# Performance work log

Hardware: AMD Instinct MI355X
Metric: run time of the kernel (lower is better)

## Reference

```python
import jax, jax.numpy as jnp
import numpy as np

TEMP = 0.07
HARD_K = 512
EMB_D = 768
PROJ_D = 128
QUEUE = 32768
BATCH = 2048
NUM_CLASSES = 2


def setup_inputs() -> dict:
    key = jax.random.key(0)
    ks = jax.random.split(key, 8)
    embeddings = jax.random.normal(ks[0], (BATCH, EMB_D), dtype=jnp.float32)
    labels = jax.random.randint(ks[1], (BATCH,), 0, NUM_CLASSES)
    # projector params: Linear(D,D) -> ReLU -> Linear(D,128)
    W1 = jax.random.normal(ks[2], (EMB_D, EMB_D), dtype=jnp.float32) * 0.02
    b1 = jnp.zeros((EMB_D,), dtype=jnp.float32)
    W2 = jax.random.normal(ks[3], (EMB_D, PROJ_D), dtype=jnp.float32) * 0.02
    b2 = jnp.zeros((PROJ_D,), dtype=jnp.float32)
    # queue buffers: L2-normalized random embeddings (as in __init__) with valid labels
    qe = jax.random.normal(ks[4], (QUEUE, PROJ_D), dtype=jnp.float32)
    queue_embeddings = qe / jnp.linalg.norm(qe, axis=1, keepdims=True)
    queue_labels = jax.random.randint(ks[5], (QUEUE,), 0, NUM_CLASSES)
    return {
        'embeddings': embeddings, 'labels': labels,
        'W1': W1, 'b1': b1, 'W2': W2, 'b2': b2,
        'queue_embeddings': queue_embeddings, 'queue_labels': queue_labels,
    }


def reference(embeddings, labels, W1, b1, W2, b2, queue_embeddings, queue_labels):
    n = embeddings.shape[0]
    # projector + L2 normalize
    h = jax.nn.relu(embeddings @ W1 + b1)
    z = h @ W2 + b2
    z = z / jnp.linalg.norm(z, axis=1, keepdims=True)  # (N, 128)

    # pairwise in-batch similarities, scaled by temperature
    S = (z @ z.T) / TEMP  # (N, N)
    same = labels[:, None] == labels[None, :]
    eye = jnp.eye(n, dtype=bool)
    pos_mask = same & ~eye           # positives: same label, not self
    neg_mask = ~same                 # in-batch negatives: different label

    # logsumexp over in-batch negatives per anchor (-inf rows -> -inf, handled by logaddexp)
    neg_batch = jnp.where(neg_mask, S, -jnp.inf)
    lse_batch = jax.scipy.special.logsumexp(neg_batch, axis=1)  # (N,)

    # hard negatives from queue: opposite-label, top-K by similarity
    sims_q = z @ queue_embeddings.T  # (N, Q)
    opp = (queue_labels[None, :] != labels[:, None]) & (queue_labels[None, :] >= 0)
    masked_q = jnp.where(opp, sims_q, -jnp.inf)
    topk_vals, _ = jax.lax.top_k(masked_q, HARD_K)  # (N, K); -inf pads drop from logsumexp
    # fallback (no opposite-label entries): first K queue embeddings regardless of label
    fallback = sims_q[:, :HARD_K]
    has_opp = opp.any(axis=1, keepdims=True)
    neg_q = jnp.where(has_opp, topk_vals, fallback) / TEMP
    lse_queue = jax.scipy.special.logsumexp(neg_q, axis=1)  # (N,)

    # all negatives for anchor i: batch negatives ++ queue hard negatives
    lse_neg = jnp.logaddexp(lse_batch, lse_queue)  # (N,)

    # per positive pair (i, j): log_prob = pos_sim - logsumexp([pos_sim, negs])
    log_prob = S - jnp.logaddexp(S, lse_neg[:, None])  # (N, N)
    losses = jnp.where(pos_mask, -log_prob, 0.0)
    count = pos_mask.sum()
    return jnp.where(count > 0, losses.sum() / count.astype(losses.dtype), 0.0)
```

## Files before the change

kernel.cpp:

```cpp
#include <hip/hip_runtime.h>
#include <hip/hip_fp16.h>

#define BATCH_N   2048
#define EMB_D_    768
#define PROJ_D_   128
#define QUEUE_N   32768
#define HARD_K_   512
static constexpr float INV_T  = 1.0f / 0.07f;
static constexpr float WLO    = 0.12f;
static constexpr float S8ENC  = 255.0f / 0.88f;
static constexpr float BINW   = 0.88f / 255.0f;

typedef __attribute__((ext_vector_type(8))) short short8;
typedef __attribute__((ext_vector_type(4))) short short4v;
typedef __attribute__((ext_vector_type(4))) float f32x4;

__device__ __forceinline__ unsigned short f2bf(float f) {
    unsigned u = __float_as_uint(f);
    unsigned r = u + 0x7fffu + ((u >> 16) & 1u);
    return (unsigned short)(r >> 16);
}
__device__ __forceinline__ float bf2f(short s) {
    return __uint_as_float(((unsigned)(unsigned short)s) << 16);
}
__device__ __forceinline__ int opp_of(int mylab, const int* __restrict__ qcnt) {
    const int same = (mylab == 0) ? qcnt[0] : ((mylab == 1) ? qcnt[1] : 0);
    return qcnt[2] - same;
}

__global__ void __launch_bounds__(256) prep(const float* __restrict__ emb, short* __restrict__ embb,
                                            const float* __restrict__ queue, short* __restrict__ qb,
                                            const int* __restrict__ qlab, int* __restrict__ qpart,
                                            const float* __restrict__ W1, short* __restrict__ w1t,
                                            const float* __restrict__ W2, short* __restrict__ w2t,
                                            const int* __restrict__ labels, int* __restrict__ rcnt,
                                            int* __restrict__ pc) {
    __shared__ float tile[64][65];
    const int b = blockIdx.x, t = threadIdx.x;
    if (b < 1536) {
        const int i = b * 256 + t;
        const float4 f = ((const float4*)emb)[i];
        short4v o = {(short)f2bf(f.x), (short)f2bf(f.y), (short)f2bf(f.z), (short)f2bf(f.w)};
        ((short4v*)embb)[i] = o;
    } else if (b < 5632) {
        const int i = (b - 1536) * 256 + t;
        const float4 f = ((const float4*)queue)[i];
        short4v o = {(short)f2bf(f.x), (short)f2bf(f.y), (short)f2bf(f.z), (short)f2bf(f.w)};
        ((short4v*)qb)[i] = o;
    } else if (b < 5664) {
        const int i = (b - 5632) * 256 + t;
        int c0 = 0, c1 = 0, cv = 0;
        for (int j = i; j < QUEUE_N; j += 8192) {
            const int q = qlab[j];
            c0 += (q == 0); c1 += (q == 1); cv += (q >= 0);
        }
        #pragma unroll
        for (int o = 32; o > 0; o >>= 1) {
            c0 += __shfl_xor(c0, o); c1 += __shfl_xor(c1, o); cv += __shfl_xor(cv, o);
        }
        int* red = (int*)tile;
        const int wv = t >> 6;
        if ((t & 63) == 0) { red[wv * 4 + 0] = c0; red[wv * 4 + 1] = c1; red[wv * 4 + 2] = cv; }
        __syncthreads();
        if (t == 0) {
            const int bb = (b - 5632) * 4;
            qpart[bb + 0] = red[0] + red[4] + red[8]  + red[12];
            qpart[bb + 1] = red[1] + red[5] + red[9]  + red[13];
            qpart[bb + 2] = red[2] + red[6] + red[10] + red[14];
        }
    } else if (b < 5832) {
        const int bid = b - 5664;
        const float* A; short* At; int R, C, bx, by;
        if (bid < 144) { A = W1; At = w1t; R = EMB_D_; C = EMB_D_;  bx = (bid % 12) * 64; by = (bid / 12) * 64; }
        else { const int b2 = bid - 144; A = W2; At = w2t; R = EMB_D_; C = PROJ_D_; bx = (b2 & 1) * 64; by = (b2 >> 1) * 64; }
        const int tc = t & 63, tg = t >> 6;
        #pragma unroll
        for (int i = 0; i < 16; i++) {
            const int r = tg * 16 + i;
            tile[r][tc] = A[(size_t)(by + r) * C + bx + tc];
        }
        __syncthreads();
        #pragma unroll
        for (int i = 0; i < 16; i++) {
            const int r = tg * 16 + i;
            At[(size_t)(bx + r) * R + by + tc] = (short)f2bf(tile[tc][r]);
        }
    } else {
        int c = 0;
        for (int j = t; j < BATCH_N; j += 256) c += (labels[j] == 0);
        #pragma unroll
        for (int o = 32; o > 0; o >>= 1) c += __shfl_xor(c, o);
        int* red = (int*)tile;
        if ((t & 63) == 0) red[t >> 6] = c;
        __syncthreads();
        if (t == 0) rcnt[0] = red[0] + red[1] + red[2] + red[3];
        if (t < 8) pc[t] = 0;
    }
}

__global__ void __launch_bounds__(256) mfma_h64(const short* __restrict__ Ab,
                                                const short* __restrict__ Bb,
                                                const float* __restrict__ bias,
                                                short* __restrict__ C,
                                                int N, int K) {
    __shared__ __align__(16) short As[64 * 128];
    __shared__ __align__(16) short Bs[128 * 128];
    const int t = threadIdx.x;
    const int lane = t & 63, wv = t >> 6;
    const int l16 = lane & 15, l4 = lane >> 4;
    const int m0 = blockIdx.y * 64, n0 = blockIdx.x * 128;
    const int wn = wv * 32;

    f32x4 acc[4][2];
    #pragma unroll
    for (int i = 0; i < 4; ++i)
        #pragma unroll
        for (int j = 0; j < 2; ++j) acc[i][j] = f32x4{0.f, 0.f, 0.f, 0.f};

    for (int kb = 0; kb < K; kb += 128) {
        __syncthreads();
        #pragma unroll
        for (int it = 0; it < 4; ++it) {
            const int r = it * 4 + wv, row = r * 4 + l4, cg = l16 ^ (row & 15);
            __builtin_amdgcn_global_load_lds(
                (const __attribute__((address_space(1))) void*)(Ab + (size_t)(m0 + row) * K + kb + cg * 8),
                (__attribute__((address_space(3))) void*)(As + r * 512), 16, 0, 0);
        }
        #pragma unroll
        for (int it = 0; it < 8; ++it) {
            const int r = it * 4 + wv, row = r * 4 + l4, cg = l16 ^ (row & 15);
            __builtin_amdgcn_global_load_lds(
                (const __attribute__((address_space(1))) void*)(Bb + (size_t)(n0 + row) * K + kb + cg * 8),
                (__attribute__((address_space(3))) void*)(Bs + r * 512), 16, 0, 0);
        }
        __syncthreads();
        #pragma unroll
        for (int ks = 0; ks < 4; ++ks) {
            short8 af[4], bfr[2];
            const int ch = (ks * 4 + l4) ^ l16;
            #pragma unroll
            for (int i = 0; i < 4; ++i)
                af[i] = *(const short8*)(As + (i * 16 + l16) * 128 + ch * 8);
            #pragma unroll
            for (int j = 0; j < 2; ++j)
                bfr[j] = *(const short8*)(Bs + (wn + j * 16 + l16) * 128 + ch * 8);
            #pragma unroll
            for (int i = 0; i < 4; ++i)
                #pragma unroll
                for (int j = 0; j < 2; ++j)
                    acc[i][j] = __builtin_amdgcn_mfma_f32_16x16x32_bf16(af[i], bfr[j], acc[i][j], 0, 0, 0);
        }
    }

    float bsv[2];
    #pragma unroll
    for (int j = 0; j < 2; ++j) bsv[j] = bias[n0 + wn + j * 16 + l16];
    #pragma unroll
    for (int i = 0; i < 4; ++i)
        #pragma unroll
        for (int r = 0; r < 4; ++r) {
            const int m = m0 + i * 16 + l4 * 4 + r;
            #pragma unroll
            for (int j = 0; j < 2; ++j) {
                const int n = n0 + wn + j * 16 + l16;
                const float v = fmaxf(acc[i][j][r] + bsv[j], 0.0f);
                C[(size_t)m * N + n] = (short)f2bf(v);
            }
        }
}

__global__ void __launch_bounds__(256) znorm_perm(const short* __restrict__ Ab,
                                                  const short* __restrict__ Bb,
                                                  const float* __restrict__ bias,
                                                  short* __restrict__ zb,
                                                  const int* __restrict__ qlab,
                                                  const int* __restrict__ labels,
                                                  const int* __restrict__ qpart,
                                                  const int* __restrict__ rcnt,
                                                  int* __restrict__ qcnt,
                                                  int* __restrict__ colidx,
                                                  int* __restrict__ qlabp,
                                                  int* __restrict__ rowmap,
                                                  int* __restrict__ rlabp,
                                                  int* __restrict__ pc) {
    __shared__ __align__(16) short As[32 * 128];
    __shared__ __align__(16) short Bs[128 * 128];
    __shared__ float ssq[32];
    __shared__ int wcnt[4][3];
    __shared__ int gbase[3];
    const int blk = blockIdx.x;
    const int t = threadIdx.x;
    const int lane = t & 63, wv = t >> 6;

    if (blk >= 64) {
        const unsigned long long below = (1ull << lane) - 1ull;
        int q0 = 0, q1 = 0, qv = 0;
        for (int i = 0; i < 32; ++i) {
            q0 += qpart[i * 4]; q1 += qpart[i * 4 + 1]; qv += qpart[i * 4 + 2];
        }
        if (blk < 192) {
            const int cb = blk - 64;
            if (cb == 0 && t == 0) { qcnt[0] = q0; qcnt[1] = q1; qcnt[2] = qv; }
            const int j = cb * 256 + t;
            const int q = qlab[j];
            const int cls = (q == 0) ? 0 : ((q == 1) ? 1 : 2);
            const unsigned long long b0 = __ballot(cls == 0);
            const unsigned long long b1 = __ballot(cls == 1);
            const unsigned long long b2 = __ballot(cls == 2);
            const int rank = (cls == 0) ? __popcll(b0 & below)
                           : ((cls == 1) ? __popcll(b1 & below) : __popcll(b2 & below));
            if (lane == 0) {
                wcnt[wv][0] = __popcll(b0); wcnt[wv][1] = __popcll(b1); wcnt[wv][2] = __popcll(b2);
            }
            __syncthreads();
            if (t < 3) {
                const int tot = wcnt[0][t] + wcnt[1][t] + wcnt[2][t] + wcnt[3][t];
                gbase[t] = atomicAdd(&pc[t], tot);
            }
            __syncthreads();
            int wb = 0;
            #pragma unroll
            for (int w = 0; w < 4; ++w) if (w < wv) wb += wcnt[w][cls];
            const int cbase = (cls == 0) ? 0 : ((cls == 1) ? q0 : q0 + q1);
            const int pos = cbase + gbase[cls] + wb + rank;
            colidx[pos] = j; qlabp[pos] = q;
        } else {
            const int r = (blk - 192) * 256 + t;
            const int l = labels[r];
            const int cls = (l == 0) ? 0 : 1;
            const unsigned long long b0 = __ballot(cls == 0);
            const unsigned long long b1 = __ballot(cls == 1);
            const int rank = (cls == 0) ? __popcll(b0 & below) : __popcll(b1 & below);
            if (lane == 0) { wcnt[wv][0] = __popcll(b0); wcnt[wv][1] = __popcll(b1); }
            __syncthreads();
            if (t < 2) {
                const int tot = wcnt[0][t] + wcnt[1][t] + wcnt[2][t] + wcnt[3][t];
                gbase[t] = atomicAdd(&pc[3 + t], tot);
            }
            __syncthreads();
            int wb = 0;
            #pragma unroll
            for (int w = 0; w < 4; ++w) if (w < wv) wb += wcnt[w][cls];
            const int cbase = (cls == 0) ? 0 : rcnt[0];
            const int pos = cbase + gbase[cls] + wb + rank;
            rowmap[pos] = r; rlabp[pos] = l;
        }
        return;
    }

    const int l16 = lane & 15, l4 = lane >> 4;
    const int m0 = blk * 32;
    const int wn = wv * 32;
    const int K = EMB_D_;

    if (t < 32) ssq[t] = 0.0f;

    f32x4 acc[2][2];
    #pragma unroll
    for (int i = 0; i < 2; ++i)
        #pragma unroll
        for (int j = 0; j < 2; ++j) acc[i][j] = f32x4{0.f, 0.f, 0.f, 0.f};

    for (int kb = 0; kb < K; kb += 128) {
        __syncthreads();
        #pragma unroll
        for (int it = 0; it < 2; ++it) {
            const int r = it * 4 + wv, row = r * 4 + l4, cg = l16 ^ (row & 15);
            __builtin_amdgcn_global_load_lds(
                (const __attribute__((address_space(1))) void*)(Ab + (size_t)(m0 + row) * K + kb + cg * 8),
                (__attribute__((address_space(3))) void*)(As + r * 512), 16, 0, 0);
        }
        #pragma unroll
        for (int it = 0; it < 8; ++it) {
            const int r = it * 4 + wv, row = r * 4 + l4, cg = l16 ^ (row & 15);
            __builtin_amdgcn_global_load_lds(
                (const __attribute__((address_space(1))) void*)(Bb + (size_t)(row) * K + kb + cg * 8),
                (__attribute__((address_space(3))) void*)(Bs + r * 512), 16, 0, 0);
        }
        __syncthreads();
        #pragma unroll
        for (int ks = 0; ks < 4; ++ks) {
            short8 af[2], bfr[2];
            const int ch = (ks * 4 + l4) ^ l16;
            #pragma unroll
            for (int i = 0; i < 2; ++i)
                af[i] = *(const short8*)(As + (i * 16 + l16) * 128 + ch * 8);
            #pragma unroll
            for (int j = 0; j < 2; ++j)
                bfr[j] = *(const short8*)(Bs + (wn + j * 16 + l16) * 128 + ch * 8);
            #pragma unroll
            for (int i = 0; i < 2; ++i)
                #pragma unroll
                for (int j = 0; j < 2; ++j)
                    acc[i][j] = __builtin_amdgcn_mfma_f32_16x16x32_bf16(af[i], bfr[j], acc[i][j], 0, 0, 0);
        }
    }

    float bsv[2];
    #pragma unroll
    for (int j = 0; j < 2; ++j) bsv[j] = bias[wn + j * 16 + l16];
    #pragma unroll
    for (int i = 0; i < 2; ++i)
        #pragma unroll
        for (int r = 0; r < 4; ++r) {
            float p = 0.0f;
            #pragma unroll
            for (int j = 0; j < 2; ++j) {
                acc[i][j][r] += bsv[j];
                p += acc[i][j][r] * acc[i][j][r];
            }
            #pragma unroll
            for (int o = 8; o > 0; o >>= 1) p += __shfl_xor(p, o);
            if (l16 == 0) atomicAdd(&ssq[i * 16 + l4 * 4 + r], p);
        }
    __syncthreads();
    #pragma unroll
    for (int i = 0; i < 2; ++i)
        #pragma unroll
        for (int r = 0; r < 4; ++r) {
            const int lrow = i * 16 + l4 * 4 + r;
            const float inv = rsqrtf(ssq[lrow]);
            #pragma unroll
            for (int j = 0; j < 2; ++j)
                zb[(size_t)(m0 + lrow) * PROJ_D_ + wn + j * 16 + l16] =
                    (short)f2bf(acc[i][j][r] * inv);
        }
}

__global__ void __launch_bounds__(256) mask8_spack(const short* __restrict__ zb,
                                                   const short* __restrict__ qb,
                                                   unsigned char* __restrict__ codes,
                                                   const int* __restrict__ rlabp,
                                                   const int* __restrict__ qlabp,
                                                   const int* __restrict__ colidx,
                                                   const int* __restrict__ rowmap,
                                                   const int* __restrict__ qcnt,
                                                   const int* __restrict__ rcnt,
                                                   short* __restrict__ Sbuf) {
    __shared__ __align__(16) short As[64 * 128];
    __shared__ __align__(16) short Bs[128 * 128];
    const int bid = blockIdx.x, t = threadIdx.x;
    const int lane = t & 63, wv = t >> 6;
    const int l16 = lane & 15, l4 = lane >> 4;
    const int wm = (wv & 1) * 32, wn = (wv >> 1) * 64;

    if (bid >= 2048) {
        const int q = bid - 2048;
        const int m0 = (q >> 4) * 64, n0 = (q & 15) * 128;
        #pragma unroll
        for (int it = 0; it < 4; ++it) {
            const int r = it * 4 + wv, row = r * 4 + l4, cg = l16 ^ (row & 15);
            __builtin_amdgcn_global_load_lds(
                (const __attribute__((address_space(1))) void*)(zb + (size_t)(m0 + row) * 128 + cg * 8),
                (__attribute__((address_space(3))) void*)(As + r * 512), 16, 0, 0);
        }
        #pragma unroll
        for (int it = 0; it < 8; ++it) {
            const int r = it * 4 + wv, row = r * 4 + l4, cg = l16 ^ (row & 15);
            __builtin_amdgcn_global_load_lds(
                (const __attribute__((address_space(1))) void*)(zb + (size_t)(n0 + row) * 128 + cg * 8),
                (__attribute__((address_space(3))) void*)(Bs + r * 512), 16, 0, 0);
        }
        __syncthreads();

        f32x4 acc[2][4];
        #pragma unroll
        for (int i = 0; i < 2; ++i)
            #pragma unroll
            for (int j = 0; j < 4; ++j) acc[i][j] = f32x4{0.f, 0.f, 0.f, 0.f};

        #pragma unroll
        for (int ks = 0; ks < 4; ++ks) {
            short8 af[2], bfr[4];
            const int ch = (ks * 4 + l4) ^ l16;
            #pragma unroll
            for (int i = 0; i < 2; ++i)
                af[i]  = *(const short8*)(As + (wm + i * 16 + l16) * 128 + ch * 8);
            #pragma unroll
            for (int j = 0; j < 4; ++j)
                bfr[j] = *(const short8*)(Bs + (wn + j * 16 + l16) * 128 + ch * 8);
            #pragma unroll
            for (int i = 0; i < 2; ++i)
                #pragma unroll
                for (int j = 0; j < 4; ++j)
                    acc[i][j] = __builtin_amdgcn_mfma_f32_16x16x32_bf16(af[i], bfr[j], acc[i][j], 0, 0, 0);
        }
        #pragma unroll
        for (int i = 0; i < 2; ++i)
            #pragma unroll
            for (int r = 0; r < 4; ++r) {
                const int m = m0 + wm + i * 16 + l4 * 4 + r;
                union { unsigned short u[4]; uint2 d; } pk;
                #pragma unroll
                for (int j = 0; j < 4; ++j) pk.u[j] = f2bf(acc[i][j][r]);
                *(uint2*)(Sbuf + (size_t)m * BATCH_N + n0 + wn + l16 * 4) = pk.d;
            }
        return;
    }

    const int bx = bid & 63, by = bid >> 6;
    const int m0 = by * 64;
    const int c0 = qcnt[0], c1v = qcnt[1], r0 = rcnt[0];
    int lo, hi;
    if (m0 + 64 <= r0)  { lo = c0; hi = c0 + c1v; }
    else if (m0 >= r0)  { lo = 0;  hi = c0; }
    else                { lo = 0;  hi = c0 + c1v; }
    const int bs = bx * 512;
    if (bs + 512 <= lo || bs >= hi) return;

    int ra[4], ca[32], la[8], qa[16];
    #pragma unroll
    for (int it = 0; it < 4; ++it)
        ra[it] = rowmap[m0 + (it * 4 + wv) * 4 + l4];
    #pragma unroll
    for (int tt = 0; tt < 4; ++tt)
        #pragma unroll
        for (int it = 0; it < 8; ++it)
            ca[tt * 8 + it] = colidx[bs + tt * 128 + (it * 4 + wv) * 4 + l4];
    #pragma unroll
    for (int i = 0; i < 2; ++i)
        #pragma unroll
        for (int r = 0; r < 4; ++r)
            la[i * 4 + r] = rlabp[m0 + wm + i * 16 + l4 * 4 + r];
    #pragma unroll
    for (int tt = 0; tt < 4; ++tt)
        #pragma unroll
        for (int j = 0; j < 4; ++j)
            qa[tt * 4 + j] = qlabp[bs + tt * 128 + wn + j * 16 + l16];

    #pragma unroll
    for (int it = 0; it < 4; ++it) {
        const int r = it * 4 + wv, row = r * 4 + l4, cg = l16 ^ (row & 15);
        __builtin_amdgcn_global_load_lds(
            (const __attribute__((address_space(1))) void*)(zb + (size_t)ra[it] * 128 + cg * 8),
            (__attribute__((address_space(3))) void*)(As + r * 512), 16, 0, 0);
    }
    #pragma unroll
    for (int it = 0; it < 8; ++it) {
        const int r = it * 4 + wv, row = r * 4 + l4, cg = l16 ^ (row & 15);
        __builtin_amdgcn_global_load_lds(
            (const __attribute__((address_space(1))) void*)(qb + (size_t)ca[it] * 128 + cg * 8),
            (__attribute__((address_space(3))) void*)(Bs + r * 512), 16, 0, 0);
    }
    const float C0 = 1.0f - WLO * S8ENC;
    __syncthreads();

    #pragma unroll
    for (int tt = 0; tt < 4; ++tt) {
        const int n0 = bs + tt * 128;

        f32x4 acc[2][4];
        #pragma unroll
        for (int i = 0; i < 2; ++i)
            #pragma unroll
            for (int j = 0; j < 4; ++j) acc[i][j] = f32x4{0.f, 0.f, 0.f, 0.f};

        #pragma unroll
        for (int ks = 0; ks < 4; ++ks) {
            short8 af[2], bfr[4];
            const int ch = (ks * 4 + l4) ^ l16;
            #pragma unroll
            for (int i = 0; i < 2; ++i)
                af[i]  = *(const short8*)(As + (wm + i * 16 + l16) * 128 + ch * 8);
            #pragma unroll
            for (int j = 0; j < 4; ++j)
                bfr[j] = *(const short8*)(Bs + (wn + j * 16 + l16) * 128 + ch * 8);
            #pragma unroll
            for (int i = 0; i < 2; ++i)
                #pragma unroll
                for (int j = 0; j < 4; ++j)
                    acc[i][j] = __builtin_amdgcn_mfma_f32_16x16x32_bf16(af[i], bfr[j], acc[i][j], 0, 0, 0);
        }

        if (tt < 3) {
            __syncthreads();
            #pragma unroll
            for (int it = 0; it < 8; ++it) {
                const int r = it * 4 + wv, row = r * 4 + l4, cg = l16 ^ (row & 15);
                __builtin_amdgcn_global_load_lds(
                    (const __attribute__((address_space(1))) void*)(qb + (size_t)ca[(tt + 1) * 8 + it] * 128 + cg * 8),
                    (__attribute__((address_space(3))) void*)(Bs + r * 512), 16, 0, 0);
            }
        }

        float a0[4], a1[4];
        #pragma unroll
        for (int j = 0; j < 4; ++j) {
            const int q = qa[tt * 4 + j];
            a0[j] = (q >= 0 && q != 0) ? C0 : -1e9f;
            a1[j] = (q >= 0 && q != 1) ? C0 : -1e9f;
        }
        #pragma unroll
        for (int i = 0; i < 2; ++i) {
            #pragma unroll
            for (int r = 0; r < 4; ++r) {
                const int m  = m0 + wm + i * 16 + l4 * 4 + r;
                const bool z = (la[i * 4 + r] == 0);
                unsigned pk = 0;
                #pragma unroll
                for (int j = 0; j < 4; ++j) {
                    const float add = z ? a0[j] : a1[j];
                    const float f = fmaf(acc[i][j][r], S8ENC, add);
#if __has_builtin(__builtin_amdgcn_cvt_pk_u8_f32)
                    pk = __builtin_amdgcn_cvt_pk_u8_f32(f, j, pk);
#else
                    const unsigned c = (unsigned)fminf(fmaxf(f, 0.0f), 255.0f);
                    pk |= c << (8 * j);
#endif
                }
                *(unsigned*)(codes + (size_t)m * QUEUE_N + n0 + wn + l16 * 4) = pk;
            }
        }
        if (tt < 3) __syncthreads();
    }
}

__device__ __forceinline__ void find_crossing(int* hist, int* grp, int target,
                                              int* s_bin, int* s_chi) {
    const int t = threadIdx.x;
    const int b0 = hist[4*t], b1 = hist[4*t+1], b2 = hist[4*t+2], b3 = hist[4*t+3];
    grp[t] = b0 + b1 + b2 + b3;
    __syncthreads();
    for (int off = 1; off < 256; off <<= 1) {
        int add = (t + off < 256) ? grp[t + off] : 0;
        __syncthreads();
        grp[t] += add;
        __syncthreads();
    }
    int cab = (t < 255) ? grp[t + 1] : 0;
    const int hb[4] = {b0, b1, b2, b3};
    #pragma unroll
    for (int i = 3; i >= 0; i--) {
        const int h = hb[i];
        if (cab < target && cab + h >= target) { *s_bin = 4*t + i; *s_chi = cab; }
        cab += h;
    }
    __syncthreads();
}

#define FOR_ALL_VALS(BODY)                                                   \
    _Pragma("unroll")                                                        \
    for (int _k = 0; _k < 64; _k++) {                                        \
        const float2 _f = __half22float2(*(const __half2*)&dv[_k]);          \
        { const float v = _f.x; BODY }                                       \
        { const float v = _f.y; BODY }                                       \
    }

__global__ void __launch_bounds__(256) tail_row(const unsigned char* __restrict__ codes,
                                                const int* __restrict__ qcnt,
                                                const int* __restrict__ rlabp,
                                                const int* __restrict__ rowmap,
                                                const short* __restrict__ zb,
                                                const short* __restrict__ qb,
                                                const int* __restrict__ qlab,
                                                const short* __restrict__ S,
                                                const int* __restrict__ labels,
                                                float* __restrict__ part_out,
                                                int* __restrict__ cnt_out) {
    __shared__ int hist4[1024];
    __shared__ int grp[256];
    __shared__ float zrow[128];
    __shared__ int s_bin, s_chi, s_bin2, s_chi2;
    __shared__ float scf[4];
    __shared__ int sci[4];
    __shared__ float s_Lq;
    const int p = blockIdx.x, t = threadIdx.x;
    const int orig  = rowmap[p];
    const int myLab = rlabp[p];
    const int opp   = opp_of(myLab, qcnt);

    bool have = false;
    if (opp >= HARD_K_) {
        for (int k = t; k < 1024; k += 256) hist4[k] = 0;
        __syncthreads();

        const int c0 = qcnt[0];
        const int lo = (myLab == 0) ? c0 : 0;
        const int hi = (myLab == 0) ? c0 + qcnt[1] : c0;
        const int klo = (lo & ~511) >> 4;
        const int khi = ((hi + 511) & ~511) >> 4;

        int* myh = hist4 + (t >> 6) * 256;
        const uint4* rowp = (const uint4*)(codes + (size_t)p * QUEUE_N);
        for (int k = klo + t; k < khi; k += 256) {
            const uint4 u = rowp[k];
            const unsigned w[4] = {u.x, u.y, u.z, u.w};
            #pragma unroll
            for (int q = 0; q < 4; q++)
                #pragma unroll
                for (int s = 0; s < 4; s++) {
                    const int c = (w[q] >> (8 * s)) & 0xFF;
                    if (c) atomicAdd(&myh[c], 1);
                }
        }
        __syncthreads();
        const int h = hist4[t] + hist4[256 + t] + hist4[512 + t] + hist4[768 + t];
        grp[t] = h;
        __syncthreads();
        for (int off = 1; off < 256; off <<= 1) {
            int add = (t + off < 256) ? grp[t + off] : 0;
            __syncthreads();
            grp[t] += add;
            __syncthreads();
        }
        const int total = grp[1];
        have = (total >= HARD_K_);
        if (have) {
            {
                const int above = (t < 255) ? grp[t + 1] : 0;
                if (grp[t] >= HARD_K_ && above < HARD_K_) s_bin = t;
            }
            __syncthreads();
            const int b = s_bin;

            float e = 0.0f;
            if (t > b && h) e = (float)h * __expf((WLO + ((float)t - 0.5f) * BINW - 1.0f) * INV_T);
            #pragma unroll
            for (int o = 32; o > 0; o >>= 1) e += __shfl_xor(e, o);
            if ((t & 63) == 0) scf[t >> 6] = e;
            __syncthreads();
            if (t == 0) {
                const float Eab  = scf[0] + scf[1] + scf[2] + scf[3];
                const int   cab  = (b < 255) ? grp[b + 1] : 0;
                const float ebin = __expf((WLO + ((float)b - 0.5f) * BINW - 1.0f) * INV_T);
                const float sadj = Eab + (float)(HARD_K_ - cab) * ebin;
                s_Lq = INV_T + __logf(sadj);
            }
        } else {
            __syncthreads();
        }
    }

    if (!have) {
        int* fh = hist4;
        if (t < 128) zrow[t] = bf2f(zb[(size_t)orig * 128 + t]);
        __syncthreads();

        const int mylab = myLab;
        unsigned dv[64];
        float rm = -1e30f, rs = 0.0f;
        for (int k = 0; k < 128; k++) {
            const int j = t + 256 * k;
            float d = 0.0f;
            #pragma unroll
            for (int c = 0; c < 16; ++c) {
                const short8 qv = *(const short8*)(qb + (size_t)j * 128 + c * 8);
                #pragma unroll
                for (int e = 0; e < 8; ++e) d += zrow[c * 8 + e] * bf2f(qv[e]);
            }
            if (j < HARD_K_) {
                const float sv = d * INV_T;
                if (sv > rm) { rs = rs * __expf(rm - sv) + 1.0f; rm = sv; }
                else         { rs += __expf(sv - rm); }
            }
            const int q = qlab[j];
            const float mv = (q != mylab && q >= 0) ? d : -65504.0f;
            const __half h = __float2half(mv);
            unsigned short* pp = (unsigned short*)&dv[k >> 1];
            pp[k & 1] = *(const unsigned short*)&h;
        }

        if (opp == 0) {
            float rm2 = rm, rs2 = rs;
            #pragma unroll
            for (int o = 32; o > 0; o >>= 1) {
                const float om = __shfl_xor(rm2, o), os = __shfl_xor(rs2, o);
                const float nm = fmaxf(rm2, om);
                rs2 = rs2 * __expf(rm2 - nm) + os * __expf(om - nm);
                rm2 = nm;
            }
            if ((t & 63) == 0) { scf[t >> 6] = rm2; ((float*)sci)[t >> 6] = rs2; }
            __syncthreads();
            if (t == 0) {
                float M = -1e30f, Sx = 0.0f;
                for (int w = 0; w < 4; w++) {
                    const float nm = fmaxf(M, scf[w]);
                    Sx = Sx * __expf(M - nm) + ((float*)sci)[w] * __expf(scf[w] - nm);
                    M = nm;
                }
                s_Lq = M + __logf(Sx);
            }
        } else if (opp < HARD_K_) {
            float mm = -1e30f, ss = 0.0f;
            FOR_ALL_VALS(
                if (v > -60000.0f) {
                    const float sv = v * INV_T;
                    if (sv > mm) { ss = ss * __expf(mm - sv) + 1.0f; mm = sv; }
                    else         { ss += __expf(sv - mm); }
                } )
            #pragma unroll
            for (int o = 32; o > 0; o >>= 1) {
                const float om = __shfl_xor(mm, o), os = __shfl_xor(ss, o);
                const float nm = fmaxf(mm, om);
                ss = ss * __expf(mm - nm) + os * __expf(om - nm);
                mm = nm;
            }
            if ((t & 63) == 0) { scf[t >> 6] = mm; ((float*)sci)[t >> 6] = ss; }
            __syncthreads();
            if (t == 0) {
                float M = -1e30f, Sx = 0.0f;
                for (int w = 0; w < 4; w++) {
                    const float nm = fmaxf(M, scf[w]);
                    Sx = Sx * __expf(M - nm) + ((float*)sci)[w] * __expf(scf[w] - nm);
                    M = nm;
                }
                s_Lq = M + __logf(Sx);
            }
        } else {
            float mloc = -1e30f;
            FOR_ALL_VALS( mloc = fmaxf(mloc, v); )
            #pragma unroll
            for (int o = 32; o > 0; o >>= 1) mloc = fmaxf(mloc, __shfl_xor(mloc, o));
            if ((t & 63) == 0) scf[t >> 6] = mloc;
            __syncthreads();
            const float m = fmaxf(fmaxf(scf[0], scf[1]), fmaxf(scf[2], scf[3]));

            int c1 = 0, c2 = 0;
            const float w1 = m - 0.25f, w2 = m - 1.0f;
            FOR_ALL_VALS( c1 += (v >= w1); c2 += (v >= w2); )
            #pragma unroll
            for (int o = 32; o > 0; o >>= 1) { c1 += __shfl_xor(c1, o); c2 += __shfl_xor(c2, o); }
            if ((t & 63) == 0) { sci[t >> 6] = c1; }
            __syncthreads();
            const int C1 = sci[0] + sci[1] + sci[2] + sci[3];
            __syncthreads();
            if ((t & 63) == 0) { sci[t >> 6] = c2; }
            __syncthreads();
            const int C2 = sci[0] + sci[1] + sci[2] + sci[3];

            float lo;
            if      (C1 >= HARD_K_) lo = w1;
            else if (C2 >= HARD_K_) lo = w2;
            else                    lo = -1.01f;
            const float range = m - lo;
            const float scale = 1024.0f / range;

            for (int k = t; k < 1024; k += 256) fh[k] = 0;
            __syncthreads();
            FOR_ALL_VALS(
                if (v >= lo) {
                    const float bf = fminf((v - lo) * scale, 1023.0f);
                    atomicAdd(&fh[(int)bf], 1);
                } )
            __syncthreads();
            find_crossing(fh, grp, HARD_K_, &s_bin, &s_chi);
            const int   bin1 = s_bin, chi1 = s_chi;
            const float binw = range * (1.0f / 1024.0f);
            const float lo1  = lo + bin1 * binw;
            const float ssc  = 1024.0f / binw;

            for (int k = t; k < 1024; k += 256) fh[k] = 0;
            __syncthreads();
            FOR_ALL_VALS(
                if (v >= lo) {
                    const float bf = fminf((v - lo) * scale, 1023.0f);
                    if ((int)bf == bin1) {
                        const float sf = fminf(fmaxf((v - lo1) * ssc, 0.0f), 1023.0f);
                        atomicAdd(&fh[(int)sf], 1);
                    }
                } )
            __syncthreads();
            find_crossing(fh, grp, HARD_K_ - chi1, &s_bin2, &s_chi2);
            const float thr = lo1 + s_bin2 * (binw * (1.0f / 1024.0f));

            float sl = 0.0f; int cg = 0;
            FOR_ALL_VALS( if (v > thr) { cg++; sl += __expf((v - m) * INV_T); } )
            #pragma unroll
            for (int o = 32; o > 0; o >>= 1) { sl += __shfl_xor(sl, o); cg += __shfl_xor(cg, o); }
            if ((t & 63) == 0) { scf[t >> 6] = sl; sci[t >> 6] = cg; }
            __syncthreads();
            if (t == 0) {
                const float slt = scf[0] + scf[1] + scf[2] + scf[3];
                const int   cgt = sci[0] + sci[1] + sci[2] + sci[3];
                const float sadj = slt + ((float)HARD_K_ - (float)cgt) * __expf((thr - m) * INV_T);
                s_Lq = m * INV_T + __logf(sadj);
            }
        }
    }
    __syncthreads();

    if (t >= 64) return;
    const int lane = t;
    const uint4* rp = (const uint4*)(S + (size_t)orig * BATCH_N);

    float v[32]; int lb[32];
    #pragma unroll
    for (int kk = 0; kk < 4; kk++) {
        const uint4 u = rp[lane + 64 * kk];
        const unsigned w[4] = {u.x, u.y, u.z, u.w};
        const int base = (lane + 64 * kk) * 8;
        #pragma unroll
        for (int q = 0; q < 4; q++) {
            v[kk * 8 + 2 * q]     = __uint_as_float(w[q] << 16);
            v[kk * 8 + 2 * q + 1] = __uint_as_float(w[q] & 0xFFFF0000u);
            const int i0 = base + 2 * q, i1 = base + 2 * q + 1;
            lb[kk * 8 + 2 * q]     = labels[(i0 & ~63) + ((i0 & 3) << 4) + ((i0 >> 2) & 15)];
            lb[kk * 8 + 2 * q + 1] = labels[(i1 & ~63) + ((i1 & 3) << 4) + ((i1 >> 2) & 15)];
        }
    }

    const float REF = INV_T;
    float sneg = 0.0f;
    #pragma unroll
    for (int k = 0; k < 32; k++) {
        const float ev = __expf(v[k] * INV_T - REF);
        sneg += (lb[k] != myLab) ? ev : 0.0f;
    }
    #pragma unroll
    for (int o = 32; o > 0; o >>= 1) sneg += __shfl_xor(sneg, o);
    const float lseb = (sneg > 0.0f) ? REF + __logf(sneg) : -1e30f;
    const float Lq = s_Lq;
    const float mx0 = fmaxf(lseb, Lq), mn0 = fminf(lseb, Lq);
    const float L = mx0 + __logf(1.0f + __expf(mn0 - mx0));

    float part = 0.0f; int cnt = 0;
    #pragma unroll
    for (int k = 0; k < 32; k++) {
        const int idx = ((lane + 64 * (k >> 3)) * 8) + (k & 7);
        const int col = (idx & ~63) + ((idx & 3) << 4) + ((idx >> 2) & 15);
        if (lb[k] == myLab && col != orig) {
            const float sv = v[k] * INV_T;
            const float mx = fmaxf(sv, L), mn = fminf(sv, L);
            part += (mx - sv) + __logf(1.0f + __expf(mn - mx));
            cnt++;
        }
    }
    #pragma unroll
    for (int o = 32; o > 0; o >>= 1) { part += __shfl_xor(part, o); cnt += __shfl_xor(cnt, o); }
    if (lane == 0) { part_out[orig] = part; cnt_out[orig] = cnt; }
}

__global__ void __launch_bounds__(256) finalize_loss(const float* __restrict__ part,
                                                     const int* __restrict__ cnt,
                                                     float* __restrict__ out) {
    const int t = threadIdx.x;
    float s = 0.0f; int c = 0;
    #pragma unroll
    for (int k = 0; k < 8; k++) { s += part[t + 256 * k]; c += cnt[t + 256 * k]; }
    #pragma unroll
    for (int o = 32; o > 0; o >>= 1) { s += __shfl_xor(s, o); c += __shfl_xor(c, o); }
    __shared__ float sf[4]; __shared__ int sc[4];
    if ((t & 63) == 0) { sf[t >> 6] = s; sc[t >> 6] = c; }
    __syncthreads();
    if (t == 0) {
        const float st = sf[0] + sf[1] + sf[2] + sf[3];
        const int   ct = sc[0] + sc[1] + sc[2] + sc[3];
        out[0] = (ct > 0) ? (st / (float)ct) : 0.0f;
    }
}

extern "C" void kernel_launch(void* const* d_in, const int* in_sizes, int n_in,
                              void* d_out, int out_size, void* d_ws, size_t ws_size,
                              hipStream_t stream) {
    const float* emb    = (const float*)d_in[0];
    const int*   labels = (const int*)  d_in[1];
    const float* W1     = (const float*)d_in[2];
    const float* b1     = (const float*)d_in[3];
    const float* W2     = (const float*)d_in[4];
    const float* b2     = (const float*)d_in[5];
    const float* queue  = (const float*)d_in[6];
    const int*   qlab   = (const int*)  d_in[7];

    char* ws = (char*)d_ws;
    short*         Sbuf  = (short*)        (ws);
    unsigned char* codes = (unsigned char*)(ws + 16777216);
    short*         embb  = (short*)        (ws + 83886080);
    short*         hbf   = (short*)        (ws + 87031808);
    short*         zb    = (short*)        (ws + 90177536);
    short*         qb    = (short*)        (ws + 90701824);
    short*         w1t   = (short*)        (ws + 99090432);
    short*         w2t   = (short*)        (ws + 100270080);
    int*           qcnt  = (int*)          (ws + 100474880);
    int*           rcnt  = (int*)          (ws + 100474944);
    int*           pc    = (int*)          (ws + 100475008);
    int*           qpart = (int*)          (ws + 100475072);
    float*         partb = (float*)        (ws + 100475584);
    int*           cntb  = (int*)          (ws + 100483776);
    int*           colidx= (int*)          (ws + 100491968);
    int*           qlabp = (int*)          (ws + 100623040);
    int*           rowmap= (int*)          (ws + 100754112);
    int*           rlabp = (int*)          (ws + 100762304);

    dim3 blk(256);
    prep<<<dim3(5833), blk, 0, stream>>>(emb, embb, queue, qb, qlab, qpart, W1, w1t, W2, w2t, labels, rcnt, pc);
    mfma_h64<<<dim3(EMB_D_ / 128, BATCH_N / 64), blk, 0, stream>>>(embb, w1t, b1, hbf, EMB_D_, EMB_D_);
    znorm_perm<<<dim3(200), blk, 0, stream>>>(hbf, w2t, b2, zb, qlab, labels, qpart, rcnt,
                                              qcnt, colidx, qlabp, rowmap, rlabp, pc);
    mask8_spack<<<dim3(2560), blk, 0, stream>>>(zb, qb, codes, rlabp, qlabp, colidx, rowmap, qcnt, rcnt, Sbuf);
    tail_row<<<dim3(BATCH_N), blk, 0, stream>>>(codes, qcnt, rlabp, rowmap, zb, qb, qlab,
                                                Sbuf, labels, partb, cntb);
    finalize_loss<<<1, blk, 0, stream>>>(partb, cntb, (float*)d_out);
}
```

Baseline: 155.0 us.

## Double-buffer LDS tiles in projector GEMM kernels to overlap loads with MFMA

Result: no change. 156.6 us (+1.0%).

```diff
diff --git a/kernel.cpp b/kernel.cpp
--- a/kernel.cpp
+++ b/kernel.cpp
@@ -103,8 +103,8 @@
                                                 const float* __restrict__ bias,
                                                 short* __restrict__ C,
                                                 int N, int K) {
-    __shared__ __align__(16) short As[64 * 128];
-    __shared__ __align__(16) short Bs[128 * 128];
+    __shared__ __align__(16) short As[2 * 64 * 128];
+    __shared__ __align__(16) short Bs[2 * 128 * 128];
     const int t = threadIdx.x;
     const int lane = t & 63, wv = t >> 6;
     const int l16 = lane & 15, l4 = lane >> 4;
@@ -117,39 +117,62 @@
         #pragma unroll
         for (int j = 0; j < 2; ++j) acc[i][j] = f32x4{0.f, 0.f, 0.f, 0.f};
 
-    for (int kb = 0; kb < K; kb += 128) {
-        __syncthreads();
-        #pragma unroll
-        for (int it = 0; it < 4; ++it) {
-            const int r = it * 4 + wv, row = r * 4 + l4, cg = l16 ^ (row & 15);
-            __builtin_amdgcn_global_load_lds(
-                (const __attribute__((address_space(1))) void*)(Ab + (size_t)(m0 + row) * K + kb + cg * 8),
-                (__attribute__((address_space(3))) void*)(As + r * 512), 16, 0, 0);
-        }
-        #pragma unroll
-        for (int it = 0; it < 8; ++it) {
-            const int r = it * 4 + wv, row = r * 4 + l4, cg = l16 ^ (row & 15);
-            __builtin_amdgcn_global_load_lds(
-                (const __attribute__((address_space(1))) void*)(Bb + (size_t)(n0 + row) * K + kb + cg * 8),
-                (__attribute__((address_space(3))) void*)(Bs + r * 512), 16, 0, 0);
-        }
-        __syncthreads();
+    const int nk = K >> 7;
+    #pragma unroll
+    for (int it = 0; it < 4; ++it) {
+        const int r = it * 4 + wv, row = r * 4 + l4, cg = l16 ^ (row & 15);
+        __builtin_amdgcn_global_load_lds(
+            (const __attribute__((address_space(1))) void*)(Ab + (size_t)(m0 + row) * K + cg * 8),
+            (__attribute__((address_space(3))) void*)(As + r * 512), 16, 0, 0);
+    }
+    #pragma unroll
+    for (int it = 0; it < 8; ++it) {
+        const int r = it * 4 + wv, row = r * 4 + l4, cg = l16 ^ (row & 15);
+        __builtin_amdgcn_global_load_lds(
+            (const __attribute__((address_space(1))) void*)(Bb + (size_t)(n0 + row) * K + cg * 8),
+            (__attribute__((address_space(3))) void*)(Bs + r * 512), 16, 0, 0);
+    }
+    __syncthreads();
+
+    for (int ki = 0; ki < nk; ++ki) {
+        const int cur = ki & 1;
+        if (ki + 1 < nk) {
+            const int kb = (ki + 1) << 7;
+            const int nb = cur ^ 1;
+            #pragma unroll
+            for (int it = 0; it < 4; ++it) {
+                const int r = it * 4 + wv, row = r * 4 + l4, cg = l16 ^ (row & 15);
+                __builtin_amdgcn_global_load_lds(
+                    (const __attribute__((address_space(1))) void*)(Ab + (size_t)(m0 + row) * K + kb + cg * 8),
+                    (__attribute__((address_space(3))) void*)(As + nb * 8192 + r * 512), 16, 0, 0);
+            }
+            #pragma unroll
+            for (int it = 0; it < 8; ++it) {
+                const int r = it * 4 + wv, row = r * 4 + l4, cg = l16 ^ (row & 15);
+                __builtin_amdgcn_global_load_lds(
+                    (const __attribute__((address_space(1))) void*)(Bb + (size_t)(n0 + row) * K + kb + cg * 8),
+                    (__attribute__((address_space(3))) void*)(Bs + nb * 16384 + r * 512), 16, 0, 0);
+            }
+        }
+        const short* Ac = As + cur * 8192;
+        const short* Bc = Bs + cur * 16384;
         #pragma unroll
         for (int ks = 0; ks < 4; ++ks) {
             short8 af[4], bfr[2];
             const int ch = (ks * 4 + l4) ^ l16;
             #pragma unroll
             for (int i = 0; i < 4; ++i)
-                af[i] = *(const short8*)(As + (i * 16 + l16) * 128 + ch * 8);
+                af[i] = *(const short8*)(Ac + (i * 16 + l16) * 128 + ch * 8);
             #pragma unroll
             for (int j = 0; j < 2; ++j)
-                bfr[j] = *(const short8*)(Bs + (wn + j * 16 + l16) * 128 + ch * 8);
+                bfr[j] = *(const short8*)(Bc + (wn + j * 16 + l16) * 128 + ch * 8);
             #pragma unroll
             for (int i = 0; i < 4; ++i)
                 #pragma unroll
                 for (int j = 0; j < 2; ++j)
                     acc[i][j] = __builtin_amdgcn_mfma_f32_16x16x32_bf16(af[i], bfr[j], acc[i][j], 0, 0, 0);
         }
+        __syncthreads();
     }
 
     float bsv[2];
@@ -183,8 +206,8 @@
                                                   int* __restrict__ rowmap,
                                                   int* __restrict__ rlabp,
                                                   int* __restrict__ pc) {
-    __shared__ __align__(16) short As[32 * 128];
-    __shared__ __align__(16) short Bs[128 * 128];
+    __shared__ __align__(16) short As[2 * 32 * 128];
+    __shared__ __align__(16) short Bs[2 * 128 * 128];
     __shared__ float ssq[32];
     __shared__ int wcnt[4][3];
     __shared__ int gbase[3];
@@ -261,39 +284,62 @@
         #pragma unroll
         for (int j = 0; j < 2; ++j) acc[i][j] = f32x4{0.f, 0.f, 0.f, 0.f};
 
-    for (int kb = 0; kb < K; kb += 128) {
-        __syncthreads();
-        #pragma unroll
-        for (int it = 0; it < 2; ++it) {
-            const int r = it * 4 + wv, row = r * 4 + l4, cg = l16 ^ (row & 15);
-            __builtin_amdgcn_global_load_lds(
-                (const __attribute__((address_space(1))) void*)(Ab + (size_t)(m0 + row) * K + kb + cg * 8),
-                (__attribute__((address_space(3))) void*)(As + r * 512), 16, 0, 0);
-        }
-        #pragma unroll
-        for (int it = 0; it < 8; ++it) {
-            const int r = it * 4 + wv, row = r * 4 + l4, cg = l16 ^ (row & 15);
-            __builtin_amdgcn_global_load_lds(
-                (const __attribute__((address_space(1))) void*)(Bb + (size_t)(row) * K + kb + cg * 8),
-                (__attribute__((address_space(3))) void*)(Bs + r * 512), 16, 0, 0);
-        }
-        __syncthreads();
+    const int nk = K >> 7;
+    #pragma unroll
+    for (int it = 0; it < 2; ++it) {
+        const int r = it * 4 + wv, row = r * 4 + l4, cg = l16 ^ (row & 15);
+        __builtin_amdgcn_global_load_lds(
+            (const __attribute__((address_space(1))) void*)(Ab + (size_t)(m0 + row) * K + cg * 8),
+            (__attribute__((address_space(3))) void*)(As + r * 512), 16, 0, 0);
+    }
+    #pragma unroll
+    for (int it = 0; it < 8; ++it) {
+        const int r = it * 4 + wv, row = r * 4 + l4, cg = l16 ^ (row & 15);
+        __builtin_amdgcn_global_load_lds(
+            (const __attribute__((address_space(1))) void*)(Bb + (size_t)(row) * K + cg * 8),
+            (__attribute__((address_space(3))) void*)(Bs + r * 512), 16, 0, 0);
+    }
+    __syncthreads();
+
+    for (int ki = 0; ki < nk; ++ki) {
+        const int cur = ki & 1;
+        if (ki + 1 < nk) {
+            const int kb = (ki + 1) << 7;
+            const int nb = cur ^ 1;
+            #pragma unroll
+            for (int it = 0; it < 2; ++it) {
+                const int r = it * 4 + wv, row = r * 4 + l4, cg = l16 ^ (row & 15);
+                __builtin_amdgcn_global_load_lds(
+                    (const __attribute__((address_space(1))) void*)(Ab + (size_t)(m0 + row) * K + kb + cg * 8),
+                    (__attribute__((address_space(3))) void*)(As + nb * 4096 + r * 512), 16, 0, 0);
+            }
+            #pragma unroll
+            for (int it = 0; it < 8; ++it) {
+                const int r = it * 4 + wv, row = r * 4 + l4, cg = l16 ^ (row & 15);
+                __builtin_amdgcn_global_load_lds(
+                    (const __attribute__((address_space(1))) void*)(Bb + (size_t)(row) * K + kb + cg * 8),
+                    (__attribute__((address_space(3))) void*)(Bs + nb * 16384 + r * 512), 16, 0, 0);
+            }
+        }
+        const short* Ac = As + cur * 4096;
+        const short* Bc = Bs + cur * 16384;
         #pragma unroll
         for (int ks = 0; ks < 4; ++ks) {
             short8 af[2], bfr[2];
             const int ch = (ks * 4 + l4) ^ l16;
             #pragma unroll
             for (int i = 0; i < 2; ++i)
-                af[i] = *(const short8*)(As + (i * 16 + l16) * 128 + ch * 8);
+                af[i] = *(const short8*)(Ac + (i * 16 + l16) * 128 + ch * 8);
             #pragma unroll
             for (int j = 0; j < 2; ++j)
-                bfr[j] = *(const short8*)(Bs + (wn + j * 16 + l16) * 128 + ch * 8);
+                bfr[j] = *(const short8*)(Bc + (wn + j * 16 + l16) * 128 + ch * 8);
             #pragma unroll
             for (int i = 0; i < 2; ++i)
                 #pragma unroll
                 for (int j = 0; j < 2; ++j)
                     acc[i][j] = __builtin_amdgcn_mfma_f32_16x16x32_bf16(af[i], bfr[j], acc[i][j], 0, 0, 0);
         }
+        __syncthreads();
     }
 
     float bsv[2];
```
